# Performance work log

Hardware: AMD Instinct MI355X
Metric: run time of the kernel (lower is better)

Reference implementation:

```python
import jax, jax.numpy as jnp
import numpy as np

SOBEL_X = jnp.array([[-1., 0., 1.], [-2., 0., 2.], [-1., 0., 1.]], dtype=jnp.float32).reshape(1, 1, 3, 3)
SOBEL_Y = jnp.array([[-1., -2., -1.], [0., 0., 0.], [1., 2., 1.]], dtype=jnp.float32).reshape(1, 1, 3, 3)
KERNEL_MASK = jnp.ones((1, 1, 3, 3), dtype=jnp.float32)


def _conv(x, k):
    # x: (N,1,H,W), k: (1,1,3,3), SAME padding (matches torch padding=1)
    return jax.lax.conv_general_dilated(
        x, k, window_strides=(1, 1), padding='SAME',
        dimension_numbers=('NCHW', 'OIHW', 'NCHW'))


def setup_inputs() -> dict:
    key = jax.random.key(0)
    k1, k2, k3 = jax.random.split(key, 3)
    shape = (2, 6, 512, 512, 8)  # (B, T, H, W, F)
    prediction = jax.random.normal(k1, shape, dtype=jnp.float32)
    target = jax.random.normal(k2, shape, dtype=jnp.float32)
    mask = jax.random.randint(k3, shape, 0, 2, dtype=jnp.int32)
    return {"prediction": prediction, "target": target, "mask": mask}


def reference(prediction, target, mask):
    B, T, H, W, F = prediction.shape
    # (B,T,H,W,F) -> (B*T*F, 1, H, W)
    def to_nchw(x):
        return x.transpose(0, 1, 4, 2, 3).reshape(B * T * F, 1, H, W)

    mask_r = to_nchw(mask.astype(jnp.float32))
    pred_r = to_nchw(prediction)
    tgt_r = to_nchw(target)

    valid = (_conv(mask_r, KERNEL_MASK) == 9.0).astype(prediction.dtype)

    gx_p = _conv(pred_r, SOBEL_X) * valid
    gy_p = _conv(pred_r, SOBEL_Y) * valid
    gx_t = _conv(tgt_r, SOBEL_X) * valid
    gy_t = _conv(tgt_r, SOBEL_Y) * valid

    # mode == 'l1'
    loss = jnp.abs(gx_p - gx_t) + jnp.abs(gy_p - gy_t)
    # (B*T*F,1,H,W) -> (B,T,H,W,F)
    return loss.reshape(B, T, F, H, W).transpose(0, 1, 3, 4, 2)
```

## Files before the change

kernel.cpp:

```cpp
#include <hip/hip_runtime.h>


constexpr int H = 512, W = 512, F = 8;
constexpr int IMAGES = 12;
constexpr int NB = IMAGES * H * 4;

typedef float f32x4 __attribute__((ext_vector_type(4)));

__global__ __launch_bounds__(256) void sobel_loss_kernel(
    const float* __restrict__ pred,
    const float* __restrict__ tgt,
    const int*   __restrict__ mask,
    float*       __restrict__ out)
{
    const int tid  = threadIdx.x;
    const int lane = tid & 63;
    const int wid  = tid >> 6;

    const int b0  = blockIdx.x;
    const int bid = (b0 & 7) * (NB >> 3) + (b0 >> 3);

    const int img  = bid >> 11;
    const int rest = bid & 2047;
    const int r    = rest >> 2;
    const int quad = rest & 3;

    const int p = lane >> 1;
    const int q = lane & 1;
    const int w = quad * 128 + wid * 32 + p;

    const size_t ibase = (size_t)img * ((size_t)H * W * F);
    const int voff = w * F + q * 4;
    float* const orow = out + ibase + (size_t)r * (W * F) + voff;

    if (r == 0 || r == H - 1) {
        f32x4 z = {0.f, 0.f, 0.f, 0.f};
        __builtin_nontemporal_store(z, (f32x4*)orow);
        return;
    }

    const bool eL = (p == 0);
    const bool eR = (p == 31);
    const bool edge = eL || eR;
    const int  wn  = eL ? (w > 0 ? w - 1 : 0) : (w < W - 1 ? w + 1 : W - 1);
    const int  eoff = wn * F + q * 4;
    const bool win  = (w > 0) & (w < W - 1);

    const size_t ro0 = ibase + (size_t)(r - 1) * (W * F);
    const size_t ro1 = ibase + (size_t)(r    ) * (W * F);
    const size_t ro2 = ibase + (size_t)(r + 1) * (W * F);

    const float4 P0 = *(const float4*)(pred + ro0 + voff);
    const float4 P1 = *(const float4*)(pred + ro1 + voff);
    const float4 P2 = *(const float4*)(pred + ro2 + voff);
    const float4 T0 = *(const float4*)(tgt  + ro0 + voff);
    const float4 T1 = *(const float4*)(tgt  + ro1 + voff);
    const float4 T2 = *(const float4*)(tgt  + ro2 + voff);
    const int4   M0 = *(const int4*)(mask + ro0 + voff);
    const int4   M1 = *(const int4*)(mask + ro1 + voff);
    const int4   M2 = *(const int4*)(mask + ro2 + voff);

    float4 EP0, EP1, EP2, ET0, ET1, ET2;
    int4   EM0, EM1, EM2;
    EP0 = EP1 = EP2 = ET0 = ET1 = ET2 = make_float4(0.f, 0.f, 0.f, 0.f);
    EM0 = EM1 = EM2 = make_int4(0, 0, 0, 0);
    if (edge) {
        EP0 = *(const float4*)(pred + ro0 + eoff);
        EP1 = *(const float4*)(pred + ro1 + eoff);
        EP2 = *(const float4*)(pred + ro2 + eoff);
        ET0 = *(const float4*)(tgt  + ro0 + eoff);
        ET1 = *(const float4*)(tgt  + ro1 + eoff);
        ET2 = *(const float4*)(tgt  + ro2 + eoff);
        EM0 = *(const int4*)(mask + ro0 + eoff);
        EM1 = *(const int4*)(mask + ro1 + eoff);
        EM2 = *(const int4*)(mask + ro2 + eoff);
    }

#define SUB4(a, b) make_float4((a).x - (b).x, (a).y - (b).y, (a).z - (b).z, (a).w - (b).w)
#define PACK(M) ((unsigned)((M).x | ((M).y << 1) | ((M).z << 2) | ((M).w << 3)))

    float4 hx0, hx1, hx2, hs0, hs1, hs2;
    unsigned hm0, hm1, hm2;

#define ROWOP(P, T, M, EP, ET, EM, HX, HS, HM)                                \
    {                                                                         \
        const float4 d  = SUB4(P, T);                                         \
        const float4 ed = SUB4(EP, ET);                                       \
        const unsigned m  = PACK(M);                                          \
        const unsigned em = PACK(EM);                                         \
        float4 dl, dr;                                                        \
        dl.x = __shfl_up(d.x, 2);   dl.y = __shfl_up(d.y, 2);                 \
        dl.z = __shfl_up(d.z, 2);   dl.w = __shfl_up(d.w, 2);                 \
        dr.x = __shfl_down(d.x, 2); dr.y = __shfl_down(d.y, 2);               \
        dr.z = __shfl_down(d.z, 2); dr.w = __shfl_down(d.w, 2);               \
        unsigned ml = (unsigned)__shfl_up((int)m, 2);                         \
        unsigned mr = (unsigned)__shfl_down((int)m, 2);                       \
        if (eL) { dl = ed; ml = em; }                                         \
        if (eR) { dr = ed; mr = em; }                                         \
        HX = SUB4(dr, dl);                                                    \
        HS = make_float4(dl.x + 2.f * d.x + dr.x,                             \
                         dl.y + 2.f * d.y + dr.y,                             \
                         dl.z + 2.f * d.z + dr.z,                             \
                         dl.w + 2.f * d.w + dr.w);                            \
        HM = ml & m & mr;                                                     \
    }

    ROWOP(P0, T0, M0, EP0, ET0, EM0, hx0, hs0, hm0)
    ROWOP(P1, T1, M1, EP1, ET1, EM1, hx1, hs1, hm1)
    ROWOP(P2, T2, M2, EP2, ET2, EM2, hx2, hs2, hm2)

#undef ROWOP

    unsigned vm = hm0 & hm1 & hm2;
    if (!win) vm = 0u;

    f32x4 o;
    {
        const float gx = hx0.x + 2.f * hx1.x + hx2.x;
        const float gy = hs2.x - hs0.x;
        o.x = (vm & 1u) ? (fabsf(gx) + fabsf(gy)) : 0.f;
    }
    {
        const float gx = hx0.y + 2.f * hx1.y + hx2.y;
        const float gy = hs2.y - hs0.y;
        o.y = (vm & 2u) ? (fabsf(gx) + fabsf(gy)) : 0.f;
    }
    {
        const float gx = hx0.z + 2.f * hx1.z + hx2.z;
        const float gy = hs2.z - hs0.z;
        o.z = (vm & 4u) ? (fabsf(gx) + fabsf(gy)) : 0.f;
    }
    {
        const float gx = hx0.w + 2.f * hx1.w + hx2.w;
        const float gy = hs2.w - hs0.w;
        o.w = (vm & 8u) ? (fabsf(gx) + fabsf(gy)) : 0.f;
    }

    __builtin_nontemporal_store(o, (f32x4*)orow);

#undef SUB4
#undef PACK
}

extern "C" void kernel_launch(void* const* d_in, const int* in_sizes, int n_in,
                              void* d_out, int out_size, void* d_ws, size_t ws_size,
                              hipStream_t stream) {
    const float* pred = (const float*)d_in[0];
    const float* tgt  = (const float*)d_in[1];
    const int*   mask = (const int*)d_in[2];
    float*       out  = (float*)d_out;

    sobel_loss_kernel<<<NB, 256, 0, stream>>>(pred, tgt, mask, out);
}
```

Measured before the change: 317.9 us.

## Process 32-row groups per block with double-buffered row loads

Each block now walks 32 consecutive rows instead of handling one row, so the grid is 16x smaller. Loads for the next row are issued before the current row is computed, in two register buffers, to overlap memory latency. Each row still reloads all three neighbour rows with no register reuse, so global traffic is unchanged, and the fewer blocks may lower occupancy and latency hiding. Output stores switched from nontemporal to regular stores, and border rows are handled by clamping the row index and zeroing the mask.

New measurement: 339.1 us. 6.7% more time.

```diff
diff --git a/kernel.cpp b/kernel.cpp
--- a/kernel.cpp
+++ b/kernel.cpp
@@ -3,7 +3,10 @@
 
 constexpr int H = 512, W = 512, F = 8;
 constexpr int IMAGES = 12;
-constexpr int NB = IMAGES * H * 4;
+constexpr int QUADS  = 4;
+constexpr int RG     = 32;
+constexpr int NGRP   = H / RG;
+constexpr int NB     = IMAGES * QUADS * NGRP;
 
 typedef float f32x4 __attribute__((ext_vector_type(4)));
 
@@ -20,10 +23,11 @@
     const int b0  = blockIdx.x;
     const int bid = (b0 & 7) * (NB >> 3) + (b0 >> 3);
 
-    const int img  = bid >> 11;
-    const int rest = bid & 2047;
-    const int r    = rest >> 2;
-    const int quad = rest & 3;
+    const int img  = bid >> 6;
+    const int rest = bid & 63;
+    const int quad = rest >> 4;
+    const int grp  = rest & 15;
+    const int r0   = grp * RG;
 
     const int p = lane >> 1;
     const int q = lane & 1;
@@ -31,13 +35,6 @@
 
     const size_t ibase = (size_t)img * ((size_t)H * W * F);
     const int voff = w * F + q * 4;
-    float* const orow = out + ibase + (size_t)r * (W * F) + voff;
-
-    if (r == 0 || r == H - 1) {
-        f32x4 z = {0.f, 0.f, 0.f, 0.f};
-        __builtin_nontemporal_store(z, (f32x4*)orow);
-        return;
-    }
 
     const bool eL = (p == 0);
     const bool eR = (p == 31);
@@ -46,41 +43,32 @@
     const int  eoff = wn * F + q * 4;
     const bool win  = (w > 0) & (w < W - 1);
 
-    const size_t ro0 = ibase + (size_t)(r - 1) * (W * F);
-    const size_t ro1 = ibase + (size_t)(r    ) * (W * F);
-    const size_t ro2 = ibase + (size_t)(r + 1) * (W * F);
-
-    const float4 P0 = *(const float4*)(pred + ro0 + voff);
-    const float4 P1 = *(const float4*)(pred + ro1 + voff);
-    const float4 P2 = *(const float4*)(pred + ro2 + voff);
-    const float4 T0 = *(const float4*)(tgt  + ro0 + voff);
-    const float4 T1 = *(const float4*)(tgt  + ro1 + voff);
-    const float4 T2 = *(const float4*)(tgt  + ro2 + voff);
-    const int4   M0 = *(const int4*)(mask + ro0 + voff);
-    const int4   M1 = *(const int4*)(mask + ro1 + voff);
-    const int4   M2 = *(const int4*)(mask + ro2 + voff);
-
-    float4 EP0, EP1, EP2, ET0, ET1, ET2;
-    int4   EM0, EM1, EM2;
-    EP0 = EP1 = EP2 = ET0 = ET1 = ET2 = make_float4(0.f, 0.f, 0.f, 0.f);
-    EM0 = EM1 = EM2 = make_int4(0, 0, 0, 0);
-    if (edge) {
-        EP0 = *(const float4*)(pred + ro0 + eoff);
-        EP1 = *(const float4*)(pred + ro1 + eoff);
-        EP2 = *(const float4*)(pred + ro2 + eoff);
-        ET0 = *(const float4*)(tgt  + ro0 + eoff);
-        ET1 = *(const float4*)(tgt  + ro1 + eoff);
-        ET2 = *(const float4*)(tgt  + ro2 + eoff);
-        EM0 = *(const int4*)(mask + ro0 + eoff);
-        EM1 = *(const int4*)(mask + ro1 + eoff);
-        EM2 = *(const int4*)(mask + ro2 + eoff);
-    }
-
 #define SUB4(a, b) make_float4((a).x - (b).x, (a).y - (b).y, (a).z - (b).z, (a).w - (b).w)
 #define PACK(M) ((unsigned)((M).x | ((M).y << 1) | ((M).z << 2) | ((M).w << 3)))
 
-    float4 hx0, hx1, hx2, hs0, hs1, hs2;
-    unsigned hm0, hm1, hm2;
+#define DECLBUF(S) float4 P0##S, P1##S, P2##S, T0##S, T1##S, T2##S; \
+                   int4   M0##S, M1##S, M2##S;
+    DECLBUF(A)
+    DECLBUF(B)
+
+#define LOADBUF(S, R)                                                         \
+    {                                                                         \
+        const int r_ = (R);                                                   \
+        const int ra = (r_ - 1 < 0) ? 0 : r_ - 1;                             \
+        const int rc = (r_ + 1 > H - 1) ? H - 1 : r_ + 1;                     \
+        const size_t o0 = ibase + (size_t)ra * (W * F) + voff;                \
+        const size_t o1 = ibase + (size_t)r_ * (W * F) + voff;                \
+        const size_t o2 = ibase + (size_t)rc * (W * F) + voff;                \
+        P0##S = *(const float4*)(pred + o0);                                  \
+        P1##S = *(const float4*)(pred + o1);                                  \
+        P2##S = *(const float4*)(pred + o2);                                  \
+        T0##S = *(const float4*)(tgt  + o0);                                  \
+        T1##S = *(const float4*)(tgt  + o1);                                  \
+        T2##S = *(const float4*)(tgt  + o2);                                  \
+        M0##S = *(const int4*)(mask + o0);                                    \
+        M1##S = *(const int4*)(mask + o1);                                    \
+        M2##S = *(const int4*)(mask + o2);                                    \
+    }
 
 #define ROWOP(P, T, M, EP, ET, EM, HX, HS, HM)                                \
     {                                                                         \
@@ -105,41 +93,68 @@
         HM = ml & m & mr;                                                     \
     }
 
-    ROWOP(P0, T0, M0, EP0, ET0, EM0, hx0, hs0, hm0)
-    ROWOP(P1, T1, M1, EP1, ET1, EM1, hx1, hs1, hm1)
-    ROWOP(P2, T2, M2, EP2, ET2, EM2, hx2, hs2, hm2)
-
-#undef ROWOP
-
-    unsigned vm = hm0 & hm1 & hm2;
-    if (!win) vm = 0u;
-
-    f32x4 o;
-    {
-        const float gx = hx0.x + 2.f * hx1.x + hx2.x;
-        const float gy = hs2.x - hs0.x;
-        o.x = (vm & 1u) ? (fabsf(gx) + fabsf(gy)) : 0.f;
-    }
-    {
-        const float gx = hx0.y + 2.f * hx1.y + hx2.y;
-        const float gy = hs2.y - hs0.y;
-        o.y = (vm & 2u) ? (fabsf(gx) + fabsf(gy)) : 0.f;
-    }
-    {
-        const float gx = hx0.z + 2.f * hx1.z + hx2.z;
-        const float gy = hs2.z - hs0.z;
-        o.z = (vm & 4u) ? (fabsf(gx) + fabsf(gy)) : 0.f;
-    }
-    {
-        const float gx = hx0.w + 2.f * hx1.w + hx2.w;
-        const float gy = hs2.w - hs0.w;
-        o.w = (vm & 8u) ? (fabsf(gx) + fabsf(gy)) : 0.f;
+#define COMPUTE(S, R)                                                         \
+    {                                                                         \
+        const int r_ = (R);                                                   \
+        const int ra = (r_ - 1 < 0) ? 0 : r_ - 1;                             \
+        const int rc = (r_ + 1 > H - 1) ? H - 1 : r_ + 1;                     \
+        float4 EP0, EP1, EP2, ET0, ET1, ET2;                                  \
+        int4   EM0, EM1, EM2;                                                 \
+        EP0 = EP1 = EP2 = ET0 = ET1 = ET2 = make_float4(0.f, 0.f, 0.f, 0.f);  \
+        EM0 = EM1 = EM2 = make_int4(0, 0, 0, 0);                              \
+        if (edge) {                                                           \
+            const size_t e0 = ibase + (size_t)ra * (W * F) + eoff;            \
+            const size_t e1 = ibase + (size_t)r_ * (W * F) + eoff;            \
+            const size_t e2 = ibase + (size_t)rc * (W * F) + eoff;            \
+            EP0 = *(const float4*)(pred + e0);                                \
+            EP1 = *(const float4*)(pred + e1);                                \
+            EP2 = *(const float4*)(pred + e2);                                \
+            ET0 = *(const float4*)(tgt  + e0);                                \
+            ET1 = *(const float4*)(tgt  + e1);                                \
+            ET2 = *(const float4*)(tgt  + e2);                                \
+            EM0 = *(const int4*)(mask + e0);                                  \
+            EM1 = *(const int4*)(mask + e1);                                  \
+            EM2 = *(const int4*)(mask + e2);                                  \
+        }                                                                     \
+        float4 hx0, hx1, hx2, hs0, hs1, hs2;                                  \
+        unsigned hm0, hm1, hm2;                                               \
+        ROWOP(P0##S, T0##S, M0##S, EP0, ET0, EM0, hx0, hs0, hm0)              \
+        ROWOP(P1##S, T1##S, M1##S, EP1, ET1, EM1, hx1, hs1, hm1)              \
+        ROWOP(P2##S, T2##S, M2##S, EP2, ET2, EM2, hx2, hs2, hm2)              \
+        unsigned vm = hm0 & hm1 & hm2;                                        \
+        if (!win || r_ == 0 || r_ == H - 1) vm = 0u;                          \
+        f32x4 o;                                                              \
+        { const float gx = hx0.x + 2.f * hx1.x + hx2.x;                       \
+          const float gy = hs2.x - hs0.x;                                     \
+          o.x = (vm & 1u) ? (fabsf(gx) + fabsf(gy)) : 0.f; }                  \
+        { const float gx = hx0.y + 2.f * hx1.y + hx2.y;                       \
+          const float gy = hs2.y - hs0.y;                                     \
+          o.y = (vm & 2u) ? (fabsf(gx) + fabsf(gy)) : 0.f; }                  \
+        { const float gx = hx0.z + 2.f * hx1.z + hx2.z;                       \
+          const float gy = hs2.z - hs0.z;                                     \
+          o.z = (vm & 4u) ? (fabsf(gx) + fabsf(gy)) : 0.f; }                  \
+        { const float gx = hx0.w + 2.f * hx1.w + hx2.w;                       \
+          const float gy = hs2.w - hs0.w;                                     \
+          o.w = (vm & 8u) ? (fabsf(gx) + fabsf(gy)) : 0.f; }                  \
+        *(f32x4*)(out + ibase + (size_t)r_ * (W * F) + voff) = o;             \
     }
 
-    __builtin_nontemporal_store(o, (f32x4*)orow);
+    LOADBUF(A, r0)
+#pragma unroll 1
+    for (int i = 0; i < RG; i += 2) {
+        const int r = r0 + i;
+        LOADBUF(B, r + 1)
+        COMPUTE(A, r)
+        if (i + 2 < RG) LOADBUF(A, r + 2)
+        COMPUTE(B, r + 1)
+    }
 
+#undef COMPUTE
+#undef ROWOP
+#undef LOADBUF
+#undef DECLBUF
+#undef PACK
 #undef SUB4
-#undef PACK
 }
 
 extern "C" void kernel_launch(void* const* d_in, const int* in_sizes, int n_in,
```
